# Kernel optimization log

Hardware: AMD Instinct MI355X
Metric: run time of the kernel (lower is better)

The kernel has to match this reference:

```python
import jax, jax.numpy as jnp
import numpy as np

B, N, C, H = 65536, 20, 128, 4
HD = C // H  # head_dim = 32
OC = 128     # out_channels
RED = 4      # SE reduction


def setup_inputs() -> dict:
    key = jax.random.key(0)
    ks = jax.random.split(key, 12)
    def xavier(k, shape):
        fan_in, fan_out = shape[1], shape[0]
        lim = jnp.sqrt(6.0 / (fan_in + fan_out))
        return jax.random.uniform(k, shape, jnp.float32, -lim, lim)
    return {
        'x': jax.random.normal(ks[0], (B, C), jnp.float32),
        'neighbors': jax.random.normal(ks[1], (B, N, C), jnp.float32),
        'Wq': xavier(ks[2], (H * HD, C)), 'bq': jnp.zeros((H * HD,), jnp.float32),
        'Wk': xavier(ks[3], (H * HD, C)), 'bk': jnp.zeros((H * HD,), jnp.float32),
        'Wv': xavier(ks[4], (H * HD, C)), 'bv': jnp.zeros((H * HD,), jnp.float32),
        'Wo': xavier(ks[5], (OC, H * HD)), 'bo': jnp.zeros((OC,), jnp.float32),
        'Wse1': xavier(ks[6], (OC // RED, OC)),
        'Wse2': xavier(ks[7], (OC, OC // RED)),
        'Wg': xavier(ks[8], (1, C + OC)), 'bg': jnp.zeros((1,), jnp.float32),
    }


def reference(x, neighbors, Wq, bq, Wk, bk, Wv, bv, Wo, bo, Wse1, Wse2, Wg, bg):
    # QKV projections
    q = (x @ Wq.T + bq).reshape(B, H, HD)                 # [b, h, d] (single query token)
    k = (neighbors @ Wk.T + bk).reshape(B, N, H, HD)      # [b, n, h, d]
    v = (neighbors @ Wv.T + bv).reshape(B, N, H, HD)
    # attention: one query over n neighbors per head
    scores = jnp.einsum('bhd,bnhd->bhn', q, k) / jnp.sqrt(jnp.float32(HD))
    attn = jax.nn.softmax(scores, axis=-1)                # [b, h, n]
    out = jnp.einsum('bhn,bnhd->bhd', attn, v)            # [b, h, d]
    # torch does squeeze(2).permute(0,2,1).reshape(b,-1): d-major interleave of heads
    out = jnp.transpose(out, (0, 2, 1)).reshape(B, HD * H)
    out = out @ Wo.T + bo                                 # [b, out_channels]
    # SE gate (avg-pool over length-1 dim is identity)
    se = jax.nn.sigmoid(jax.nn.relu(out @ Wse1.T) @ Wse2.T)
    out = out * se
    # learned residual gate (in_channels == out_channels -> no padding)
    gate = jax.nn.sigmoid(jnp.concatenate([x, out], axis=1) @ Wg.T + bg)  # [b, 1]
    return gate * out + (1.0 - gate) * x
```

## Files before the change

kernel.cpp:

```cpp
#include <hip/hip_runtime.h>
#include <hip/hip_bf16.h>
#include <stdint.h>

#define NROWS 65536

typedef short short8 __attribute__((ext_vector_type(8)));
typedef short shortv4 __attribute__((ext_vector_type(4)));
typedef float f32x4 __attribute__((ext_vector_type(4)));

__device__ __forceinline__ short f2bf(float f) {
  uint32_t u = __float_as_uint(f);
  u += 0x7FFFu + ((u >> 16) & 1u);
  return (short)(u >> 16);
}
__device__ __forceinline__ float bf2f(short s) {
  return __uint_as_float(((uint32_t)(uint16_t)s) << 16);
}
__device__ __forceinline__ short8 pk8(float4 a, float4 b) {
  short8 r;
  r[0] = f2bf(a.x); r[1] = f2bf(a.y); r[2] = f2bf(a.z); r[3] = f2bf(a.w);
  r[4] = f2bf(b.x); r[5] = f2bf(b.y); r[6] = f2bf(b.z); r[7] = f2bf(b.w);
  return r;
}
__device__ __forceinline__ void unpack8(uint4 u, float* f) {
  f[0] = __uint_as_float(u.x << 16); f[1] = __uint_as_float(u.x & 0xFFFF0000u);
  f[2] = __uint_as_float(u.y << 16); f[3] = __uint_as_float(u.y & 0xFFFF0000u);
  f[4] = __uint_as_float(u.z << 16); f[5] = __uint_as_float(u.z & 0xFFFF0000u);
  f[6] = __uint_as_float(u.w << 16); f[7] = __uint_as_float(u.w & 0xFFFF0000u);
}

__global__ __launch_bounds__(256) void k_prep(
    const float* __restrict__ Wq, const float* __restrict__ Wk,
    const float* __restrict__ Wv, const float* __restrict__ Wo,
    const float* __restrict__ Ws1, const float* __restrict__ Ws2,
    short* __restrict__ wq, short* __restrict__ wkt, short* __restrict__ wv,
    short* __restrict__ wo, short* __restrict__ ws1, short* __restrict__ ws2)
{
  int idx = blockIdx.x * 256 + threadIdx.x;
  int stride = gridDim.x * 256;
  for (int i = idx; i < 16384; i += stride) {
    wq[i] = f2bf(Wq[i]);
    wv[i] = f2bf(Wv[i]);
    wo[i] = f2bf(Wo[i]);
    int c = i >> 7, d = i & 127;
    wkt[i] = f2bf(Wk[d * 128 + c]);
  }
  for (int i = idx; i < 4096; i += stride) {
    ws1[i] = f2bf(Ws1[i]);
    ws2[i] = f2bf(Ws2[i]);
  }
}

__global__ __launch_bounds__(256) void k_qt(
    const float* __restrict__ x, const float* __restrict__ bq,
    const short* __restrict__ wq, const short* __restrict__ wkt,
    short* __restrict__ T)
{
  __shared__ short qtile[4][16 * 136];
  const int wid = threadIdx.x >> 6;
  const int lane = threadIdx.x & 63;
  const int g = lane & 15;
  const int q4 = lane >> 4;
  const int r0 = blockIdx.x * 64 + wid * 16;
  short* Q = qtile[wid];

  short8 af[4];
#pragma unroll
  for (int ks = 0; ks < 4; ++ks) {
    const float* p = x + (size_t)(r0 + g) * 128 + ks * 32 + q4 * 8;
    af[ks] = pk8(*(const float4*)p, *(const float4*)(p + 4));
  }
#pragma unroll
  for (int nt = 0; nt < 8; ++nt) {
    f32x4 acc = {0.f, 0.f, 0.f, 0.f};
#pragma unroll
    for (int ks = 0; ks < 4; ++ks) {
      short8 bfr = *(const short8*)(wq + (nt * 16 + g) * 128 + ks * 32 + q4 * 8);
      acc = __builtin_amdgcn_mfma_f32_16x16x32_bf16(af[ks], bfr, acc, 0, 0, 0);
    }
    float bias = bq[nt * 16 + g];
#pragma unroll
    for (int i = 0; i < 4; ++i)
      Q[(q4 * 4 + i) * 136 + nt * 16 + g] = f2bf(acc[i] + bias);
  }
  __syncthreads();

#pragma unroll
  for (int h = 0; h < 4; ++h) {
    short8 a = *(const short8*)(Q + g * 136 + h * 32 + q4 * 8);
#pragma unroll
    for (int nt = 0; nt < 8; ++nt) {
      short8 bfr = *(const short8*)(wkt + (nt * 16 + g) * 128 + h * 32 + q4 * 8);
      f32x4 acc = {0.f, 0.f, 0.f, 0.f};
      acc = __builtin_amdgcn_mfma_f32_16x16x32_bf16(a, bfr, acc, 0, 0, 0);
#pragma unroll
      for (int i = 0; i < 4; ++i)
        T[(size_t)(r0 + q4 * 4 + i) * 512 + h * 128 + nt * 16 + g] = f2bf(acc[i]);
    }
  }
}

__global__ __launch_bounds__(256) void k_attn(
    const float* __restrict__ nb, short* __restrict__ TS)
{
  __shared__ short lnb[4][20 * 136];
  const int wid = threadIdx.x >> 6;
  const int lane = threadIdx.x & 63;
  const int g = lane & 15;
  const int h = lane >> 4;
  const int b = blockIdx.x * 4 + wid;
  short* L = lnb[wid];

  const float* src = nb + (size_t)b * 2560;
#pragma unroll
  for (int j = 0; j < 5; ++j) {
    int n = j * 4 + h;
    const float* p = src + n * 128 + g * 8;
    *(short8*)(L + n * 136 + g * 8) = pk8(*(const float4*)p, *(const float4*)(p + 4));
  }

  float t[8];
  unpack8(*(const uint4*)(TS + (size_t)b * 512 + h * 128 + g * 8), t);

  float sc[20];
#pragma unroll
  for (int n = 0; n < 20; ++n) {
    float c[8];
    unpack8(*(const uint4*)(L + n * 136 + g * 8), c);
    float p = t[0]*c[0] + t[1]*c[1] + t[2]*c[2] + t[3]*c[3]
            + t[4]*c[4] + t[5]*c[5] + t[6]*c[6] + t[7]*c[7];
    p += __shfl_xor(p, 1);
    p += __shfl_xor(p, 2);
    p += __shfl_xor(p, 4);
    p += __shfl_xor(p, 8);
    sc[n] = p;
  }
  float mx = sc[0];
#pragma unroll
  for (int n = 1; n < 20; ++n) mx = fmaxf(mx, sc[n]);
  const float CSC = 0.25505417705366035f;
  float sum = 0.f;
#pragma unroll
  for (int n = 0; n < 20; ++n) { sc[n] = exp2f((sc[n] - mx) * CSC); sum += sc[n]; }
  float inv = 1.f / sum;

  float s[8] = {0, 0, 0, 0, 0, 0, 0, 0};
#pragma unroll
  for (int n = 0; n < 20; ++n) {
    float c[8];
    unpack8(*(const uint4*)(L + n * 136 + g * 8), c);
#pragma unroll
    for (int k2 = 0; k2 < 8; ++k2) s[k2] += sc[n] * c[k2];
  }
  short8 o;
#pragma unroll
  for (int k2 = 0; k2 < 8; ++k2) o[k2] = f2bf(s[k2] * inv);
  *(short8*)(TS + (size_t)b * 512 + h * 128 + g * 8) = o;
}

__global__ __launch_bounds__(256) void k_out(
    const float* __restrict__ x, const short* __restrict__ S,
    const short* __restrict__ wv, const short* __restrict__ wo,
    const short* __restrict__ ws1, const short* __restrict__ ws2,
    const float* __restrict__ bv, const float* __restrict__ bo,
    const float* __restrict__ wg, const float* __restrict__ bg,
    float* __restrict__ out)
{
  __shared__ short t_ov[4][16 * 136];
  __shared__ short t_o1[4][16 * 136];
  const int wid = threadIdx.x >> 6;
  const int lane = threadIdx.x & 63;
  const int g = lane & 15;
  const int q4 = lane >> 4;
  const int r0 = blockIdx.x * 64 + wid * 16;
  short* OV = t_ov[wid];
  short* O1 = t_o1[wid];

#pragma unroll
  for (int h = 0; h < 4; ++h) {
    short8 a[4];
#pragma unroll
    for (int ks = 0; ks < 4; ++ks)
      a[ks] = *(const short8*)(S + (size_t)(r0 + g) * 512 + h * 128 + ks * 32 + q4 * 8);
#pragma unroll
    for (int nt = 0; nt < 2; ++nt) {
      f32x4 acc = {0.f, 0.f, 0.f, 0.f};
#pragma unroll
      for (int ks = 0; ks < 4; ++ks) {
        short8 bfr = *(const short8*)(wv + (h * 32 + nt * 16 + g) * 128 + ks * 32 + q4 * 8);
        acc = __builtin_amdgcn_mfma_f32_16x16x32_bf16(a[ks], bfr, acc, 0, 0, 0);
      }
      int d = nt * 16 + g;
      float bias = bv[h * 32 + d];
#pragma unroll
      for (int i = 0; i < 4; ++i)
        OV[(q4 * 4 + i) * 136 + d * 4 + h] = f2bf(acc[i] + bias);
    }
  }
  __syncthreads();

  short8 a1[4];
#pragma unroll
  for (int ks = 0; ks < 4; ++ks)
    a1[ks] = *(const short8*)(OV + g * 136 + ks * 32 + q4 * 8);
  f32x4 o1f[8];
#pragma unroll
  for (int nt = 0; nt < 8; ++nt) {
    f32x4 acc = {0.f, 0.f, 0.f, 0.f};
#pragma unroll
    for (int ks = 0; ks < 4; ++ks) {
      short8 bfr = *(const short8*)(wo + (nt * 16 + g) * 128 + ks * 32 + q4 * 8);
      acc = __builtin_amdgcn_mfma_f32_16x16x32_bf16(a1[ks], bfr, acc, 0, 0, 0);
    }
    float bias = bo[nt * 16 + g];
#pragma unroll
    for (int i = 0; i < 4; ++i) {
      acc[i] += bias;
      O1[(q4 * 4 + i) * 136 + nt * 16 + g] = f2bf(acc[i]);
    }
    o1f[nt] = acc;
  }
  __syncthreads();

  short8 a2[4];
#pragma unroll
  for (int ks = 0; ks < 4; ++ks)
    a2[ks] = *(const short8*)(O1 + g * 136 + ks * 32 + q4 * 8);
#pragma unroll
  for (int nt = 0; nt < 2; ++nt) {
    f32x4 acc = {0.f, 0.f, 0.f, 0.f};
#pragma unroll
    for (int ks = 0; ks < 4; ++ks) {
      short8 bfr = *(const short8*)(ws1 + (nt * 16 + g) * 128 + ks * 32 + q4 * 8);
      acc = __builtin_amdgcn_mfma_f32_16x16x32_bf16(a2[ks], bfr, acc, 0, 0, 0);
    }
#pragma unroll
    for (int i = 0; i < 4; ++i)
      OV[(q4 * 4 + i) * 136 + nt * 16 + g] = f2bf(fmaxf(acc[i], 0.f));
  }
  __syncthreads();

  short8 a3 = *(const short8*)(OV + g * 136 + q4 * 8);
  f32x4 sef[8];
#pragma unroll
  for (int nt = 0; nt < 8; ++nt) {
    short8 bfr = *(const short8*)(ws2 + (nt * 16 + g) * 32 + q4 * 8);
    f32x4 z4 = {0.f, 0.f, 0.f, 0.f};
    sef[nt] = __builtin_amdgcn_mfma_f32_16x16x32_bf16(a3, bfr, z4, 0, 0, 0);
  }

  const float L2E = 1.4426950408889634f;
  float wg2[8];
#pragma unroll
  for (int nt = 0; nt < 8; ++nt) wg2[nt] = wg[128 + nt * 16 + g];
  float o2v[8][4];
  float zc[4] = {0.f, 0.f, 0.f, 0.f};
#pragma unroll
  for (int nt = 0; nt < 8; ++nt)
#pragma unroll
    for (int i = 0; i < 4; ++i) {
      float se = 1.f / (1.f + exp2f(-sef[nt][i] * L2E));
      float o2 = o1f[nt][i] * se;
      o2v[nt][i] = o2;
      zc[i] += wg2[nt] * o2;
    }
#pragma unroll
  for (int i = 0; i < 4; ++i) {
    zc[i] += __shfl_xor(zc[i], 1);
    zc[i] += __shfl_xor(zc[i], 2);
    zc[i] += __shfl_xor(zc[i], 4);
    zc[i] += __shfl_xor(zc[i], 8);
  }
  float wgx[8];
#pragma unroll
  for (int j = 0; j < 8; ++j) wgx[j] = wg[g * 8 + j];
  float bgv = bg[0];
  float gate[4];
#pragma unroll
  for (int i = 0; i < 4; ++i) {
    const float* xp = x + (size_t)(r0 + q4 * 4 + i) * 128 + g * 8;
    float4 x0 = *(const float4*)xp;
    float4 x1 = *(const float4*)(xp + 4);
    float px = wgx[0]*x0.x + wgx[1]*x0.y + wgx[2]*x0.z + wgx[3]*x0.w
             + wgx[4]*x1.x + wgx[5]*x1.y + wgx[6]*x1.z + wgx[7]*x1.w;
    px += __shfl_xor(px, 1);
    px += __shfl_xor(px, 2);
    px += __shfl_xor(px, 4);
    px += __shfl_xor(px, 8);
    float z = px + zc[i] + bgv;
    gate[i] = 1.f / (1.f + exp2f(-z * L2E));
  }
#pragma unroll
  for (int nt = 0; nt < 8; ++nt)
#pragma unroll
    for (int i = 0; i < 4; ++i) {
      size_t row = r0 + q4 * 4 + i;
      float xv = x[row * 128 + nt * 16 + g];
      out[row * 128 + nt * 16 + g] = xv + gate[i] * (o2v[nt][i] - xv);
    }
}

extern "C" void kernel_launch(void* const* d_in, const int* in_sizes, int n_in,
                              void* d_out, int out_size, void* d_ws, size_t ws_size,
                              hipStream_t stream)
{
  const float* x   = (const float*)d_in[0];
  const float* nb  = (const float*)d_in[1];
  const float* Wq  = (const float*)d_in[2];
  const float* bq  = (const float*)d_in[3];
  const float* Wk  = (const float*)d_in[4];
  const float* Wv  = (const float*)d_in[6];
  const float* bv  = (const float*)d_in[7];
  const float* Wo  = (const float*)d_in[8];
  const float* bo  = (const float*)d_in[9];
  const float* Ws1 = (const float*)d_in[10];
  const float* Ws2 = (const float*)d_in[11];
  const float* wg  = (const float*)d_in[12];
  const float* bg  = (const float*)d_in[13];
  float* out = (float*)d_out;

  char* ws = (char*)d_ws;
  short* TS   = (short*)ws;
  short* wqb  = (short*)(ws + (size_t)67108864);
  short* wktb = wqb  + 16384;
  short* wvb  = wktb + 16384;
  short* wob  = wvb  + 16384;
  short* ws1b = wob  + 16384;
  short* ws2b = ws1b + 4096;

  k_prep<<<64, 256, 0, stream>>>(Wq, Wk, Wv, Wo, Ws1, Ws2,
                                 wqb, wktb, wvb, wob, ws1b, ws2b);
  k_qt  <<<1024, 256, 0, stream>>>(x, bq, wqb, wktb, TS);
  k_attn<<<16384, 256, 0, stream>>>(nb, TS);
  k_out <<<1024, 256, 0, stream>>>(x, TS, wvb, wob, ws1b, ws2b,
                                   bv, bo, wg, bg, out);
}
```

Measured before the change: 989.2 us.

## Fuse Q/T projection, attention, and output stages into one kernel

Merges the three per-row kernels into a single kernel where each 256-thread block handles 16 rows. The intermediate T/S tensors live in LDS instead of a 64 MB global workspace, which removes that round-trip traffic and two launches. The work of each matmul is split across the four waves, and each wave prefetches the next row's neighbor data while computing the current row's scores. The cost is more __syncthreads, larger LDS use per block (which may lower occupancy), and a swizzled block-to-row mapping.

```diff
diff --git a/kernel.cpp b/kernel.cpp
--- a/kernel.cpp
+++ b/kernel.cpp
@@ -1,20 +1,16 @@
 #include <hip/hip_runtime.h>
-#include <hip/hip_bf16.h>
 #include <stdint.h>
 
-#define NROWS 65536
 
 typedef short short8 __attribute__((ext_vector_type(8)));
-typedef short shortv4 __attribute__((ext_vector_type(4)));
 typedef float f32x4 __attribute__((ext_vector_type(4)));
+
+#define TSL 520
 
 __device__ __forceinline__ short f2bf(float f) {
   uint32_t u = __float_as_uint(f);
   u += 0x7FFFu + ((u >> 16) & 1u);
   return (short)(u >> 16);
-}
-__device__ __forceinline__ float bf2f(short s) {
-  return __uint_as_float(((uint32_t)(uint16_t)s) << 16);
 }
 __device__ __forceinline__ short8 pk8(float4 a, float4 b) {
   short8 r;
@@ -51,183 +47,196 @@
   }
 }
 
-__global__ __launch_bounds__(256) void k_qt(
-    const float* __restrict__ x, const float* __restrict__ bq,
+__global__ __launch_bounds__(256) void k_fused(
+    const float* __restrict__ x, const float* __restrict__ nb,
+    const float* __restrict__ bq,
     const short* __restrict__ wq, const short* __restrict__ wkt,
-    short* __restrict__ T)
-{
-  __shared__ short qtile[4][16 * 136];
-  const int wid = threadIdx.x >> 6;
-  const int lane = threadIdx.x & 63;
-  const int g = lane & 15;
-  const int q4 = lane >> 4;
-  const int r0 = blockIdx.x * 64 + wid * 16;
-  short* Q = qtile[wid];
-
-  short8 af[4];
-#pragma unroll
-  for (int ks = 0; ks < 4; ++ks) {
-    const float* p = x + (size_t)(r0 + g) * 128 + ks * 32 + q4 * 8;
-    af[ks] = pk8(*(const float4*)p, *(const float4*)(p + 4));
-  }
-#pragma unroll
-  for (int nt = 0; nt < 8; ++nt) {
-    f32x4 acc = {0.f, 0.f, 0.f, 0.f};
-#pragma unroll
-    for (int ks = 0; ks < 4; ++ks) {
-      short8 bfr = *(const short8*)(wq + (nt * 16 + g) * 128 + ks * 32 + q4 * 8);
-      acc = __builtin_amdgcn_mfma_f32_16x16x32_bf16(af[ks], bfr, acc, 0, 0, 0);
-    }
-    float bias = bq[nt * 16 + g];
-#pragma unroll
-    for (int i = 0; i < 4; ++i)
-      Q[(q4 * 4 + i) * 136 + nt * 16 + g] = f2bf(acc[i] + bias);
-  }
-  __syncthreads();
-
-#pragma unroll
-  for (int h = 0; h < 4; ++h) {
-    short8 a = *(const short8*)(Q + g * 136 + h * 32 + q4 * 8);
-#pragma unroll
-    for (int nt = 0; nt < 8; ++nt) {
-      short8 bfr = *(const short8*)(wkt + (nt * 16 + g) * 128 + h * 32 + q4 * 8);
-      f32x4 acc = {0.f, 0.f, 0.f, 0.f};
-      acc = __builtin_amdgcn_mfma_f32_16x16x32_bf16(a, bfr, acc, 0, 0, 0);
-#pragma unroll
-      for (int i = 0; i < 4; ++i)
-        T[(size_t)(r0 + q4 * 4 + i) * 512 + h * 128 + nt * 16 + g] = f2bf(acc[i]);
-    }
-  }
-}
-
-__global__ __launch_bounds__(256) void k_attn(
-    const float* __restrict__ nb, short* __restrict__ TS)
-{
-  __shared__ short lnb[4][20 * 136];
-  const int wid = threadIdx.x >> 6;
-  const int lane = threadIdx.x & 63;
-  const int g = lane & 15;
-  const int h = lane >> 4;
-  const int b = blockIdx.x * 4 + wid;
-  short* L = lnb[wid];
-
-  const float* src = nb + (size_t)b * 2560;
-#pragma unroll
-  for (int j = 0; j < 5; ++j) {
-    int n = j * 4 + h;
-    const float* p = src + n * 128 + g * 8;
-    *(short8*)(L + n * 136 + g * 8) = pk8(*(const float4*)p, *(const float4*)(p + 4));
-  }
-
-  float t[8];
-  unpack8(*(const uint4*)(TS + (size_t)b * 512 + h * 128 + g * 8), t);
-
-  float sc[20];
-#pragma unroll
-  for (int n = 0; n < 20; ++n) {
-    float c[8];
-    unpack8(*(const uint4*)(L + n * 136 + g * 8), c);
-    float p = t[0]*c[0] + t[1]*c[1] + t[2]*c[2] + t[3]*c[3]
-            + t[4]*c[4] + t[5]*c[5] + t[6]*c[6] + t[7]*c[7];
-    p += __shfl_xor(p, 1);
-    p += __shfl_xor(p, 2);
-    p += __shfl_xor(p, 4);
-    p += __shfl_xor(p, 8);
-    sc[n] = p;
-  }
-  float mx = sc[0];
-#pragma unroll
-  for (int n = 1; n < 20; ++n) mx = fmaxf(mx, sc[n]);
-  const float CSC = 0.25505417705366035f;
-  float sum = 0.f;
-#pragma unroll
-  for (int n = 0; n < 20; ++n) { sc[n] = exp2f((sc[n] - mx) * CSC); sum += sc[n]; }
-  float inv = 1.f / sum;
-
-  float s[8] = {0, 0, 0, 0, 0, 0, 0, 0};
-#pragma unroll
-  for (int n = 0; n < 20; ++n) {
-    float c[8];
-    unpack8(*(const uint4*)(L + n * 136 + g * 8), c);
-#pragma unroll
-    for (int k2 = 0; k2 < 8; ++k2) s[k2] += sc[n] * c[k2];
-  }
-  short8 o;
-#pragma unroll
-  for (int k2 = 0; k2 < 8; ++k2) o[k2] = f2bf(s[k2] * inv);
-  *(short8*)(TS + (size_t)b * 512 + h * 128 + g * 8) = o;
-}
-
-__global__ __launch_bounds__(256) void k_out(
-    const float* __restrict__ x, const short* __restrict__ S,
     const short* __restrict__ wv, const short* __restrict__ wo,
     const short* __restrict__ ws1, const short* __restrict__ ws2,
     const float* __restrict__ bv, const float* __restrict__ bo,
     const float* __restrict__ wg, const float* __restrict__ bg,
     float* __restrict__ out)
 {
-  __shared__ short t_ov[4][16 * 136];
-  __shared__ short t_o1[4][16 * 136];
-  const int wid = threadIdx.x >> 6;
+  __shared__ short U[10880];
+  __shared__ short R0[16 * TSL];
+  __shared__ float gz[4][17];
+
+  const int wid  = threadIdx.x >> 6;
   const int lane = threadIdx.x & 63;
-  const int g = lane & 15;
-  const int q4 = lane >> 4;
-  const int r0 = blockIdx.x * 64 + wid * 16;
-  short* OV = t_ov[wid];
-  short* O1 = t_o1[wid];
-
-#pragma unroll
-  for (int h = 0; h < 4; ++h) {
+  const int g    = lane & 15;
+  const int q4   = lane >> 4;
+  const int bid  = ((blockIdx.x & 7) << 9) | (blockIdx.x >> 3);
+  const int r0   = bid << 4;
+
+  short8 af[4];
+#pragma unroll
+  for (int ks = 0; ks < 4; ++ks) {
+    const float* p = x + (size_t)(r0 + g) * 128 + ks * 32 + q4 * 8;
+    af[ks] = pk8(*(const float4*)p, *(const float4*)(p + 4));
+  }
+#pragma unroll
+  for (int t2 = 0; t2 < 2; ++t2) {
+    const int nt = wid * 2 + t2;
+    f32x4 acc = {0.f, 0.f, 0.f, 0.f};
+#pragma unroll
+    for (int ks = 0; ks < 4; ++ks) {
+      short8 bfr = *(const short8*)(wq + (nt * 16 + g) * 128 + ks * 32 + q4 * 8);
+      acc = __builtin_amdgcn_mfma_f32_16x16x32_bf16(af[ks], bfr, acc, 0, 0, 0);
+    }
+    const float bias = bq[nt * 16 + g];
+#pragma unroll
+    for (int i = 0; i < 4; ++i)
+      U[(q4 * 4 + i) * 136 + nt * 16 + g] = f2bf(acc[i] + bias);
+  }
+  __syncthreads();
+
+  {
+    const int h = wid;
+    short8 a = *(const short8*)(U + g * 136 + h * 32 + q4 * 8);
+#pragma unroll
+    for (int nt = 0; nt < 8; ++nt) {
+      short8 bfr = *(const short8*)(wkt + (nt * 16 + g) * 128 + h * 32 + q4 * 8);
+      f32x4 acc = {0.f, 0.f, 0.f, 0.f};
+      acc = __builtin_amdgcn_mfma_f32_16x16x32_bf16(a, bfr, acc, 0, 0, 0);
+#pragma unroll
+      for (int i = 0; i < 4; ++i)
+        R0[(q4 * 4 + i) * TSL + h * 128 + nt * 16 + g] = f2bf(acc[i]);
+    }
+  }
+  __syncthreads();
+
+  {
+    short* L = U + wid * 2720;
+    const int h = q4;
+    const float CSC = 0.25505417705366035f;
+
+    float4 pf[10];
+    {
+      const float* src0 = nb + ((size_t)r0 + wid * 4) * 2560;
+#pragma unroll
+      for (int j = 0; j < 5; ++j) {
+        const int n = j * 4 + h;
+        const float* p = src0 + n * 128 + g * 8;
+        pf[2 * j]     = *(const float4*)p;
+        pf[2 * j + 1] = *(const float4*)(p + 4);
+      }
+    }
+
+#pragma unroll 1
+    for (int it = 0; it < 4; ++it) {
+      const int bl = wid * 4 + it;
+#pragma unroll
+      for (int j = 0; j < 5; ++j) {
+        const int n = j * 4 + h;
+        *(short8*)(L + n * 136 + g * 8) = pk8(pf[2 * j], pf[2 * j + 1]);
+      }
+      float t[8];
+      unpack8(*(const uint4*)(R0 + bl * TSL + h * 128 + g * 8), t);
+
+      float sc[20];
+#pragma unroll
+      for (int n = 0; n < 20; ++n) {
+        float c[8];
+        unpack8(*(const uint4*)(L + n * 136 + g * 8), c);
+        float p = t[0]*c[0] + t[1]*c[1] + t[2]*c[2] + t[3]*c[3]
+                + t[4]*c[4] + t[5]*c[5] + t[6]*c[6] + t[7]*c[7];
+        p += __shfl_xor(p, 1);
+        p += __shfl_xor(p, 2);
+        p += __shfl_xor(p, 4);
+        p += __shfl_xor(p, 8);
+        sc[n] = p;
+      }
+
+      if (it < 3) {
+        const float* srcn = nb + ((size_t)r0 + bl + 1) * 2560;
+#pragma unroll
+        for (int j = 0; j < 5; ++j) {
+          const int n = j * 4 + h;
+          const float* p = srcn + n * 128 + g * 8;
+          pf[2 * j]     = *(const float4*)p;
+          pf[2 * j + 1] = *(const float4*)(p + 4);
+        }
+      }
+
+      float mx = sc[0];
+#pragma unroll
+      for (int n = 1; n < 20; ++n) mx = fmaxf(mx, sc[n]);
+      float sum = 0.f;
+#pragma unroll
+      for (int n = 0; n < 20; ++n) { sc[n] = exp2f((sc[n] - mx) * CSC); sum += sc[n]; }
+      const float inv = 1.f / sum;
+
+      float s[8] = {0, 0, 0, 0, 0, 0, 0, 0};
+#pragma unroll
+      for (int n = 0; n < 20; ++n) {
+        float c[8];
+        unpack8(*(const uint4*)(L + n * 136 + g * 8), c);
+#pragma unroll
+        for (int k2 = 0; k2 < 8; ++k2) s[k2] += sc[n] * c[k2];
+      }
+      short8 o;
+#pragma unroll
+      for (int k2 = 0; k2 < 8; ++k2) o[k2] = f2bf(s[k2] * inv);
+      *(short8*)(R0 + bl * TSL + h * 128 + g * 8) = o;
+    }
+  }
+  __syncthreads();
+
+  {
+    const int h2 = wid;
     short8 a[4];
 #pragma unroll
     for (int ks = 0; ks < 4; ++ks)
-      a[ks] = *(const short8*)(S + (size_t)(r0 + g) * 512 + h * 128 + ks * 32 + q4 * 8);
+      a[ks] = *(const short8*)(R0 + g * TSL + h2 * 128 + ks * 32 + q4 * 8);
 #pragma unroll
     for (int nt = 0; nt < 2; ++nt) {
       f32x4 acc = {0.f, 0.f, 0.f, 0.f};
 #pragma unroll
       for (int ks = 0; ks < 4; ++ks) {
-        short8 bfr = *(const short8*)(wv + (h * 32 + nt * 16 + g) * 128 + ks * 32 + q4 * 8);
+        short8 bfr = *(const short8*)(wv + (h2 * 32 + nt * 16 + g) * 128 + ks * 32 + q4 * 8);
         acc = __builtin_amdgcn_mfma_f32_16x16x32_bf16(a[ks], bfr, acc, 0, 0, 0);
       }
-      int d = nt * 16 + g;
-      float bias = bv[h * 32 + d];
+      const int d = nt * 16 + g;
+      const float bias = bv[h2 * 32 + d];
 #pragma unroll
       for (int i = 0; i < 4; ++i)
-        OV[(q4 * 4 + i) * 136 + d * 4 + h] = f2bf(acc[i] + bias);
-    }
-  }
-  __syncthreads();
-
-  short8 a1[4];
-#pragma unroll
-  for (int ks = 0; ks < 4; ++ks)
-    a1[ks] = *(const short8*)(OV + g * 136 + ks * 32 + q4 * 8);
-  f32x4 o1f[8];
-#pragma unroll
-  for (int nt = 0; nt < 8; ++nt) {
-    f32x4 acc = {0.f, 0.f, 0.f, 0.f};
-#pragma unroll
-    for (int ks = 0; ks < 4; ++ks) {
-      short8 bfr = *(const short8*)(wo + (nt * 16 + g) * 128 + ks * 32 + q4 * 8);
-      acc = __builtin_amdgcn_mfma_f32_16x16x32_bf16(a1[ks], bfr, acc, 0, 0, 0);
-    }
-    float bias = bo[nt * 16 + g];
-#pragma unroll
-    for (int i = 0; i < 4; ++i) {
-      acc[i] += bias;
-      O1[(q4 * 4 + i) * 136 + nt * 16 + g] = f2bf(acc[i]);
-    }
-    o1f[nt] = acc;
-  }
-  __syncthreads();
-
-  short8 a2[4];
-#pragma unroll
-  for (int ks = 0; ks < 4; ++ks)
-    a2[ks] = *(const short8*)(O1 + g * 136 + ks * 32 + q4 * 8);
-#pragma unroll
-  for (int nt = 0; nt < 2; ++nt) {
+        U[(q4 * 4 + i) * 136 + d * 4 + h2] = f2bf(acc[i] + bias);
+    }
+  }
+  __syncthreads();
+
+  f32x4 o1f[2];
+  {
+    short8 a1[4];
+#pragma unroll
+    for (int ks = 0; ks < 4; ++ks)
+      a1[ks] = *(const short8*)(U + g * 136 + ks * 32 + q4 * 8);
+#pragma unroll
+    for (int t2 = 0; t2 < 2; ++t2) {
+      const int nt = wid * 2 + t2;
+      f32x4 acc = {0.f, 0.f, 0.f, 0.f};
+#pragma unroll
+      for (int ks = 0; ks < 4; ++ks) {
+        short8 bfr = *(const short8*)(wo + (nt * 16 + g) * 128 + ks * 32 + q4 * 8);
+        acc = __builtin_amdgcn_mfma_f32_16x16x32_bf16(a1[ks], bfr, acc, 0, 0, 0);
+      }
+      const float bias = bo[nt * 16 + g];
+#pragma unroll
+      for (int i = 0; i < 4; ++i) {
+        acc[i] += bias;
+        R0[(q4 * 4 + i) * 136 + nt * 16 + g] = f2bf(acc[i]);
+      }
+      o1f[t2] = acc;
+    }
+  }
+  __syncthreads();
+
+  if (wid < 2) {
+    short8 a2[4];
+#pragma unroll
+    for (int ks = 0; ks < 4; ++ks)
+      a2[ks] = *(const short8*)(R0 + g * 136 + ks * 32 + q4 * 8);
+    const int nt = wid;
     f32x4 acc = {0.f, 0.f, 0.f, 0.f};
 #pragma unroll
     for (int ks = 0; ks < 4; ++ks) {
@@ -236,34 +245,36 @@
     }
 #pragma unroll
     for (int i = 0; i < 4; ++i)
-      OV[(q4 * 4 + i) * 136 + nt * 16 + g] = f2bf(fmaxf(acc[i], 0.f));
-  }
-  __syncthreads();
-
-  short8 a3 = *(const short8*)(OV + g * 136 + q4 * 8);
-  f32x4 sef[8];
-#pragma unroll
-  for (int nt = 0; nt < 8; ++nt) {
-    short8 bfr = *(const short8*)(ws2 + (nt * 16 + g) * 32 + q4 * 8);
-    f32x4 z4 = {0.f, 0.f, 0.f, 0.f};
-    sef[nt] = __builtin_amdgcn_mfma_f32_16x16x32_bf16(a3, bfr, z4, 0, 0, 0);
+      U[(q4 * 4 + i) * 136 + nt * 16 + g] = f2bf(fmaxf(acc[i], 0.f));
+  }
+  __syncthreads();
+
+  f32x4 sef[2];
+  {
+    short8 a3 = *(const short8*)(U + g * 136 + q4 * 8);
+#pragma unroll
+    for (int t2 = 0; t2 < 2; ++t2) {
+      const int nt = wid * 2 + t2;
+      short8 bfr = *(const short8*)(ws2 + (nt * 16 + g) * 32 + q4 * 8);
+      f32x4 z4 = {0.f, 0.f, 0.f, 0.f};
+      sef[t2] = __builtin_amdgcn_mfma_f32_16x16x32_bf16(a3, bfr, z4, 0, 0, 0);
+    }
   }
 
   const float L2E = 1.4426950408889634f;
-  float wg2[8];
-#pragma unroll
-  for (int nt = 0; nt < 8; ++nt) wg2[nt] = wg[128 + nt * 16 + g];
-  float o2v[8][4];
+  float o2v[2][4];
   float zc[4] = {0.f, 0.f, 0.f, 0.f};
 #pragma unroll
-  for (int nt = 0; nt < 8; ++nt)
+  for (int t2 = 0; t2 < 2; ++t2) {
+    const float w2 = wg[128 + (wid * 2 + t2) * 16 + g];
 #pragma unroll
     for (int i = 0; i < 4; ++i) {
-      float se = 1.f / (1.f + exp2f(-sef[nt][i] * L2E));
-      float o2 = o1f[nt][i] * se;
-      o2v[nt][i] = o2;
-      zc[i] += wg2[nt] * o2;
-    }
+      const float se = 1.f / (1.f + exp2f(-sef[t2][i] * L2E));
+      const float o2 = o1f[t2][i] * se;
+      o2v[t2][i] = o2;
+      zc[i] += w2 * o2;
+    }
+  }
 #pragma unroll
   for (int i = 0; i < 4; ++i) {
     zc[i] += __shfl_xor(zc[i], 1);
@@ -271,14 +282,20 @@
     zc[i] += __shfl_xor(zc[i], 4);
     zc[i] += __shfl_xor(zc[i], 8);
   }
+  if (g == 0) {
+#pragma unroll
+    for (int i = 0; i < 4; ++i) gz[wid][q4 * 4 + i] = zc[i];
+  }
+  __syncthreads();
+
   float wgx[8];
 #pragma unroll
   for (int j = 0; j < 8; ++j) wgx[j] = wg[g * 8 + j];
-  float bgv = bg[0];
-  float gate[4];
+  const float bgv = bg[0];
 #pragma unroll
   for (int i = 0; i < 4; ++i) {
-    const float* xp = x + (size_t)(r0 + q4 * 4 + i) * 128 + g * 8;
+    const int row = r0 + q4 * 4 + i;
+    const float* xp = x + (size_t)row * 128 + g * 8;
     float4 x0 = *(const float4*)xp;
     float4 x1 = *(const float4*)(xp + 4);
     float px = wgx[0]*x0.x + wgx[1]*x0.y + wgx[2]*x0.z + wgx[3]*x0.w
@@ -287,17 +304,16 @@
     px += __shfl_xor(px, 2);
     px += __shfl_xor(px, 4);
     px += __shfl_xor(px, 8);
-    float z = px + zc[i] + bgv;
-    gate[i] = 1.f / (1.f + exp2f(-z * L2E));
-  }
-#pragma unroll
-  for (int nt = 0; nt < 8; ++nt)
-#pragma unroll
-    for (int i = 0; i < 4; ++i) {
-      size_t row = r0 + q4 * 4 + i;
-      float xv = x[row * 128 + nt * 16 + g];
-      out[row * 128 + nt * 16 + g] = xv + gate[i] * (o2v[nt][i] - xv);
-    }
+    const int ri = q4 * 4 + i;
+    const float z = px + gz[0][ri] + gz[1][ri] + gz[2][ri] + gz[3][ri] + bgv;
+    const float gate = 1.f / (1.f + exp2f(-z * L2E));
+#pragma unroll
+    for (int t2 = 0; t2 < 2; ++t2) {
+      const int col = (wid * 2 + t2) * 16 + g;
+      const float xv = x[(size_t)row * 128 + col];
+      out[(size_t)row * 128 + col] = xv + gate * (o2v[t2][i] - xv);
+    }
+  }
 }
 
 extern "C" void kernel_launch(void* const* d_in, const int* in_sizes, int n_in,
@@ -319,19 +335,15 @@
   const float* bg  = (const float*)d_in[13];
   float* out = (float*)d_out;
 
-  char* ws = (char*)d_ws;
-  short* TS   = (short*)ws;
-  short* wqb  = (short*)(ws + (size_t)67108864);
+  short* wqb  = (short*)d_ws;
   short* wktb = wqb  + 16384;
   short* wvb  = wktb + 16384;
   short* wob  = wvb  + 16384;
   short* ws1b = wob  + 16384;
   short* ws2b = ws1b + 4096;
 
-  k_prep<<<64, 256, 0, stream>>>(Wq, Wk, Wv, Wo, Ws1, Ws2,
-                                 wqb, wktb, wvb, wob, ws1b, ws2b);
-  k_qt  <<<1024, 256, 0, stream>>>(x, bq, wqb, wktb, TS);
-  k_attn<<<16384, 256, 0, stream>>>(nb, TS);
-  k_out <<<1024, 256, 0, stream>>>(x, TS, wvb, wob, ws1b, ws2b,
-                                   bv, bo, wg, bg, out);
-}
+  k_prep <<<64, 256, 0, stream>>>(Wq, Wk, Wv, Wo, Ws1, Ws2,
+                                  wqb, wktb, wvb, wob, ws1b, ws2b);
+  k_fused<<<4096, 256, 0, stream>>>(x, nb, bq, wqb, wktb, wvb, wob, ws1b, ws2b,
+                                    bv, bo, wg, bg, out);
+}
```

Result: faster. 963.2 us (-2.6%).
